# Kernel tuning notes

Measured on AMD Instinct MI355X. Metric: run time of the kernel, lower is better.

## Reference

```python
import jax, jax.numpy as jnp
import numpy as np
from jax import lax

FI, FO, K, EPS = 512, 256, 3, 1e-06


def _fir_kernel(gain):
    f = jnp.array([1.0, 3.0, 3.0, 1.0], dtype=jnp.float32)
    f = f[None, :] * f[:, None]
    f = f / f.sum() * gain  # (4,4), symmetric so conv-vs-correlation flip is a no-op
    return f


def setup_inputs() -> dict:
    key = jax.random.key(0)
    k1, k2 = jax.random.split(key)
    x = jax.random.normal(k1, (8, FI, 64, 64), dtype=jnp.float32)
    w = jax.random.normal(k2, (1, FO, FI, K, K), dtype=jnp.float32)
    return {"x": x, "w": w}


def reference(x, w):
    w_scale = (FI * K * K) ** (-0.5)
    wm = w[0] * w_scale  # (fo, fi, k, k); per-sample scale is constant across batch
    demod = lax.rsqrt(jnp.sum(wm * wm, axis=(1, 2, 3)) + EPS)  # (fo,)
    wm = wm * demod[:, None, None, None]
    # torch conv_transpose2d(stride=2, padding=0) with weight (fi, fo, k, k) where
    # weight[i, o] = wm[o, i]  ==  dilated conv with kernel flip(wm) OIHW, pad k-1=2.
    kern = wm[:, :, ::-1, ::-1]
    y = lax.conv_general_dilated(
        x, kern, window_strides=(1, 1), padding=[(2, 2), (2, 2)],
        lhs_dilation=(2, 2), dimension_numbers=("NCHW", "OIHW", "NCHW"))
    # upFirDn2D with scale=2, conv_k=3: p=0 -> pad (1,1) both dims, filter gain 4
    f = _fir_kernel(4.0)
    C = y.shape[1]
    fk = jnp.broadcast_to(f[None, None], (C, 1, 4, 4))
    y = lax.conv_general_dilated(
        y, fk, window_strides=(1, 1), padding=[(1, 1), (1, 1)],
        feature_group_count=C, dimension_numbers=("NCHW", "OIHW", "NCHW"))
    return y  # (8, 256, 128, 128)
```

## Files before the change

kernel.cpp:

```cpp
#include <hip/hip_runtime.h>

typedef unsigned short u16;
typedef unsigned int u32;
typedef __attribute__((ext_vector_type(8))) short bf16x8;
typedef __attribute__((ext_vector_type(4))) float f32x4;

#define XP_BYTES 35684352
#define YB_BYTES 68714544
#define HY_OFF   (XP_BYTES + YB_BYTES)
#define WS_NEED  ((size_t)HY_OFF + 2359296)
#define CS 16776

__device__ inline u16 f2bf(float f) {
  union { float f; unsigned u; } v; v.f = f;
  unsigned r = v.u + 0x7fffu + ((v.u >> 16) & 1u);
  return (u16)(r >> 16);
}

__device__ inline void gl_lds16(const u16* g, u16* l) {
  __builtin_amdgcn_global_load_lds(
      (const __attribute__((address_space(1))) unsigned int*)g,
      (__attribute__((address_space(3))) unsigned int*)l, 16, 0, 0);
}

__global__ void xprep(const float* __restrict__ x, u16* __restrict__ xp) {
  __shared__ float tile[64 * 65];
  int bid = blockIdx.x;
  int cc = bid & 7, h = (bid >> 3) & 63, n = bid >> 9;
  int c0 = cc * 64;
  int t = threadIdx.x;
  const float* xb = x + ((size_t)(n * 512 + c0) * 64 + h) * 64;
  for (int r = 0; r < 16; ++r) {
    int flat = r * 256 + t;
    int ci = flat >> 6, w = flat & 63;
    tile[w * 65 + ci] = xb[(size_t)ci * 4096 + w];
  }
  __syncthreads();
  for (int r = 0; r < 8; ++r) {
    int flat = r * 256 + t;
    int pr = flat & 31;
    int w = flat >> 5;
    int ci = pr * 2;
    float v0 = tile[w * 65 + ci], v1 = tile[w * 65 + ci + 1];
    unsigned pk = (unsigned)f2bf(v0) | ((unsigned)f2bf(v1) << 16);
    int kcabs = cc * 2 + (ci >> 5);
    int chl = ci & 31;
    u16* dst = xp + (size_t)(n * 16 + kcabs) * 139392 +
               (size_t)((h + 1) * 66 + (w + 1)) * 32 + chl;
    *(unsigned*)dst = pk;
  }
  if (t < 64) {
    int seg = t >> 4;
    int colsel = (seg >> 1) ? 65 : 0;
    int pl = cc * 2 + (seg & 1);
    int ui = t & 15;
    u16* dst = xp + (size_t)(n * 16 + pl) * 139392 +
               (size_t)((h + 1) * 66 + colsel) * 32 + ui * 2;
    *(u32*)dst = 0u;
  }
  if (h == 0 || h == 63) {
    int rowbase = (h == 0) ? 0 : 65 * 66;
    for (int j = t; j < 2112; j += 256) {
      int seg = j >> 4;
      int ui = j & 15;
      int pl = cc * 2 + (seg & 1);
      int pos = seg >> 1;
      u16* dst = xp + (size_t)(n * 16 + pl) * 139392 +
                 (size_t)(rowbase + pos) * 32 + ui * 2;
      *(u32*)dst = 0u;
    }
  }
}

__global__ void wprep9(const float* __restrict__ w, u16* __restrict__ Hy) {
  __shared__ float wl[4608];
  __shared__ float red[256];
  int o = blockIdx.x, t = threadIdx.x;
  const float* wo = w + (size_t)o * 4608;
  float s = 0.f;
  for (int j = t; j < 4608; j += 256) { float v = wo[j]; wl[j] = v; s += v * v; }
  red[t] = s;
  __syncthreads();
  for (int st = 128; st; st >>= 1) { if (t < st) red[t] += red[t + st]; __syncthreads(); }
  float demod = rsqrtf(red[0] * (1.0f / 4608.0f) + 1e-6f);
  float scale = demod * 0.014731391274719739f;
  const int DY[9] = {0, 2, 0, 2, 0, 2, 1, 1, 1};
  const int DX[9] = {0, 0, 2, 2, 1, 1, 0, 2, 1};
  for (int i = t; i < 512; i += 256) {
    int kc = i >> 5, il = i & 31;
#pragma unroll
    for (int pl = 0; pl < 9; ++pl) {
      float g = wl[i * 9 + DY[pl] * 3 + DX[pl]] * scale;
      Hy[(size_t)(pl * 16 + kc) * 8192 + (size_t)o * 32 + il] = f2bf(g);
    }
  }
}

#define BARR() __builtin_amdgcn_s_barrier()
#define WAITL() do { asm volatile("s_waitcnt lgkmcnt(0)" ::: "memory"); __builtin_amdgcn_sched_barrier(0); } while (0)
#define WAITV2() do { asm volatile("s_waitcnt vmcnt(2)" ::: "memory"); __builtin_amdgcn_sched_barrier(0); } while (0)
#define WAITV0() do { asm volatile("s_waitcnt vmcnt(0)" ::: "memory"); __builtin_amdgcn_sched_barrier(0); } while (0)

__device__ __forceinline__ void rdA4(const u16* sb, int tib, int la, int grp, int wm,
                                     bf16x8 af[4]) {
#pragma unroll
  for (int ti = 0; ti < 4; ++ti) {
    int p = (tib + ti) * 16 + la;
    int slot = (wm * 4 + grp) ^ (p & 7);
    af[ti] = *(const bf16x8*)(sb + p * 64 + slot * 8);
  }
}

__device__ __forceinline__ void rdB2(const u16* sb, int njb, int la, int grp, int wn,
                                     bf16x8 bf[2]) {
#pragma unroll
  for (int nj = 0; nj < 2; ++nj) {
    int p = (njb + nj) * 16 + la;
    int slot = (wn * 4 + grp) ^ (p & 7);
    bf[nj] = *(const bf16x8*)(sb + 8192 + p * 64 + slot * 8);
  }
}

template <int MIB, int NJ0>
__device__ __forceinline__ void qm8(const bf16x8 af[4], const bf16x8 bf[2],
                                    f32x4 acc[8][4]) {
#pragma unroll
  for (int ti = 0; ti < 4; ++ti)
#pragma unroll
    for (int nj = 0; nj < 2; ++nj)
      acc[MIB + ti][NJ0 + nj] = __builtin_amdgcn_mfma_f32_16x16x32_bf16(
          af[ti], bf[nj], acc[MIB + ti][NJ0 + nj], 0, 0, 0);
}

__device__ __forceinline__ void stA1(const u16* __restrict__ xp, u16* d,
                                     int tile, int NK, u32 a,
                                     u32 adj1, u32 adj2, u32 adj3) {
  if (tile < NK) {
    int tap = tile >> 4;
    u32 ko = (u32)((tile & 15) * 139392);
    u32 adj = tap == 0 ? 0u : (tap == 1 ? adj1 : (tap == 2 ? adj2 : adj3));
    gl_lds16(xp + (a + ko - adj), d);
  }
}

__device__ __forceinline__ void stB1(const u16* __restrict__ hb, u16* d,
                                     int tile, int NK, u32 b) {
  if (tile < NK) {
    int tap = tile >> 4;
    u32 ko = (u32)(tap * 131072 + (tile & 15) * 8192);
    gl_lds16(hb + (b + ko), d);
  }
}

__global__ __launch_bounds__(256, 2) void conv_y(const u16* __restrict__ xp,
                                                 const u16* __restrict__ Hy,
                                                 u16* __restrict__ yb) {
  __shared__ __align__(16) u16 su[24576];

  int bid = blockIdx.x;
  int t = threadIdx.x;
  int wid = t >> 6, lane = t & 63;

  int img = bid & 7;
  int kk = bid >> 3;
  int mt, oh, Wp, CNT, NTAP, PB, PO, STLIM;
  u32 adj1 = 0, adj2 = 0, adj3 = 0;
  if (kk < 34)       { int k2 = kk;       mt = k2 >> 1; oh = k2 & 1; Wp = 66; CNT = 4290; NTAP = 4; PB = 0; PO = 0;     STLIM = 4296;
                       adj1 = 2112u; adj2 = 32u; adj3 = 2144u; }
  else if (kk < 68)  { int k2 = kk - 34;  mt = k2 >> 1; oh = k2 & 1; Wp = 64; CNT = 4160; NTAP = 2; PB = 4; PO = 4296;  STLIM = 4160;
                       adj1 = 2112u; }
  else if (kk < 102) { int k2 = kk - 68;  mt = k2 >> 1; oh = k2 & 1; Wp = 66; CNT = 4224; NTAP = 2; PB = 6; PO = 8456;  STLIM = 4224;
                       adj1 = 32u; }
  else               { int k2 = kk - 102; mt = k2 >> 1; oh = k2 & 1; Wp = 64; CNT = 4096; NTAP = 1; PB = 8; PO = 12680; STLIM = 4096; }

  int m0 = mt * 256;
  int o0 = oh * 128;
  int NK = NTAP * 16;
  int NITER = NTAP * 8;
  const u16* hb = Hy + (size_t)PB * 131072;

  int wm = wid >> 1, wn = wid & 1;
  int la = lane & 15, grp = lane >> 4;

  int tp = t >> 3, ts = t & 7;
  u32 gA[4], gBv[2];
  {
    u32 ib = (u32)img * 2230272u;
#pragma unroll
    for (int j = 0; j < 4; ++j) {
      int p = j * 32 + tp;
      int e = ts ^ (p & 7);
      int ii = (e >> 2) * 128 + p;
      int kc = e & 3;
      int m = m0 + ii;
      if (m > CNT - 1) m = CNT - 1;
      u32 a = (u32)m / (u32)Wp;
      u32 b = (u32)m - a * (u32)Wp;
      gA[j] = ib + ((a + 1) * 66 + (b + 1)) * 32 + kc * 8;
    }
#pragma unroll
    for (int j = 0; j < 2; ++j) {
      int p = j * 32 + tp;
      int e = ts ^ (p & 7);
      int ol = (e >> 2) * 64 + p;
      int kc = e & 3;
      gBv[j] = (u32)((o0 + ol) * 32 + kc * 8);
    }
  }
  int ws = wid * 512;

  f32x4 acc[8][4];
#pragma unroll
  for (int i = 0; i < 8; ++i)
#pragma unroll
    for (int j = 0; j < 4; ++j) acc[i][j] = (f32x4){0.f, 0.f, 0.f, 0.f};

  stB1(hb, su + 8192 + ws, 0, NK, gBv[0]);
  stB1(hb, su + 10240 + ws, 0, NK, gBv[1]);
  stA1(xp, su + 0 + ws, 0, NK, gA[0], adj1, adj2, adj3);
  stA1(xp, su + 2048 + ws, 0, NK, gA[1], adj1, adj2, adj3);
  stA1(xp, su + 4096 + ws, 0, NK, gA[2], adj1, adj2, adj3);
  stA1(xp, su + 6144 + ws, 0, NK, gA[3], adj1, adj2, adj3);
  stB1(hb, su + 20480 + ws, 1, NK, gBv[0]);
  stB1(hb, su + 22528 + ws, 1, NK, gBv[1]);
  WAITV2();
  BARR();

  bf16x8 afA[4], afB[4], bfA[2], bfB[2];

#pragma unroll 1
  for (int it = 0; it < NITER; ++it) {
    int t0 = 2 * it;
    bool more = (it + 1 < NITER);

    rdA4(su, 0, la, grp, wm, afA);
    rdB2(su, 0, la, grp, wn, bfA);
    stA1(xp, su + 12288 + ws, t0 + 1, NK, gA[0], adj1, adj2, adj3);
    stA1(xp, su + 14336 + ws, t0 + 1, NK, gA[1], adj1, adj2, adj3);
    BARR(); WAITL();
    __builtin_amdgcn_s_setprio(1); qm8<0, 0>(afA, bfA, acc); __builtin_amdgcn_s_setprio(0);
    BARR();
    rdB2(su, 2, la, grp, wn, bfB);
    stA1(xp, su + 16384 + ws, t0 + 1, NK, gA[2], adj1, adj2, adj3);
    stA1(xp, su + 18432 + ws, t0 + 1, NK, gA[3], adj1, adj2, adj3);
    BARR(); WAITL();
    __builtin_amdgcn_s_setprio(1); qm8<0, 2>(afA, bfB, acc); __builtin_amdgcn_s_setprio(0);
    BARR();
    rdA4(su, 4, la, grp, wm, afB);
    stB1(hb, su + 8192 + ws, t0 + 2, NK, gBv[0]);
    stB1(hb, su + 10240 + ws, t0 + 2, NK, gBv[1]);
    BARR(); WAITL();
    __builtin_amdgcn_s_setprio(1);
    qm8<4, 0>(afB, bfA, acc); qm8<4, 2>(afB, bfB, acc);
    __builtin_amdgcn_s_setprio(0);
    if (more) { WAITV2(); } else { WAITV0(); }
    BARR();
    rdA4(su + 12288, 0, la, grp, wm, afA);
    rdB2(su + 12288, 0, la, grp, wn, bfA);
    stA1(xp, su + 0 + ws, t0 + 2, NK, gA[0], adj1, adj2, adj3);
    stA1(xp, su + 2048 + ws, t0 + 2, NK, gA[1], adj1, adj2, adj3);
    BARR(); WAITL();
    __builtin_amdgcn_s_setprio(1); qm8<0, 0>(afA, bfA, acc); __builtin_amdgcn_s_setprio(0);
    BARR();
    rdB2(su + 12288, 2, la, grp, wn, bfB);
    stA1(xp, su + 4096 + ws, t0 + 2, NK, gA[2], adj1, adj2, adj3);
    stA1(xp, su + 6144 + ws, t0 + 2, NK, gA[3], adj1, adj2, adj3);
    BARR(); WAITL();
    __builtin_amdgcn_s_setprio(1); qm8<0, 2>(afA, bfB, acc); __builtin_amdgcn_s_setprio(0);
    BARR();
    rdA4(su + 12288, 4, la, grp, wm, afB);
    stB1(hb, su + 20480 + ws, t0 + 3, NK, gBv[0]);
    stB1(hb, su + 22528 + ws, t0 + 3, NK, gBv[1]);
    BARR(); WAITL();
    __builtin_amdgcn_s_setprio(1);
    qm8<4, 0>(afB, bfA, acc); qm8<4, 2>(afB, bfB, acc);
    __builtin_amdgcn_s_setprio(0);
    if (more) { WAITV2(); }
    BARR();
  }

  WAITV0();
  __syncthreads();
  u16* ybp = yb + 8;
#pragma unroll 1
  for (int r = 0; r < 2; ++r) {
    if (wn == r) {
#pragma unroll
      for (int nj = 0; nj < 4; ++nj) {
        int orl = nj * 16 + la;
        int x7 = orl & 7;
#pragma unroll
        for (int mi = 0; mi < 8; ++mi)
#pragma unroll
          for (int jp = 0; jp < 2; ++jp) {
            int ml = wm * 128 + mi * 16 + grp * 4 + jp * 2;
            u32 pk = (u32)f2bf(acc[mi][nj][jp * 2]) |
                     ((u32)f2bf(acc[mi][nj][jp * 2 + 1]) << 16);
            *(u32*)(su + orl * 256 + (((ml >> 3) ^ x7) * 8) + (ml & 7)) = pk;
          }
      }
    }
    __syncthreads();
    {
      int ol = t >> 2, s2 = t & 3;
      int og = o0 + r * 64 + ol;
      size_t gb = (size_t)(img * 256 + og) * CS + PO + m0;
      int x7 = ol & 7;
#pragma unroll
      for (int i = 0; i < 8; ++i) {
        int cidx = s2 * 8 + i;
        int m = cidx * 8;
        if (m0 + m < STLIM)
          *(bf16x8*)(ybp + gb + m) = *(const bf16x8*)(su + ol * 256 + ((cidx ^ x7) * 8));
      }
    }
    if (r == 0) __syncthreads();
  }
}

__global__ void fir2(const u16* __restrict__ yb, float* __restrict__ z) {
  int flat = blockIdx.x * 256 + threadIdx.x;
  int qh = flat & 15, phb = (flat >> 4) & 31, o = (flat >> 9) & 255, n = flat >> 17;
  const u16* cb = yb + 8 + (size_t)(n * 256 + o) * CS;
  int a0 = 2 * phb - 1;
  int b0 = 4 * qh - 1;

  float out[4][8];
#pragma unroll
  for (int i = 0; i < 4; ++i)
#pragma unroll
    for (int j = 0; j < 8; ++j) out[i][j] = 0.f;

  const int PO_[4] = {0, 4296, 8456, 12680};
  const int WP_[4] = {66, 64, 66, 64};
  const int HA_[4] = {65, 65, 64, 64};
  const int WB_[4] = {65, 64, 65, 64};

#pragma unroll
  for (int ph = 0; ph < 4; ++ph) {
    int rp = ph >> 1, rq = ph & 1;
    const u16* pb = cb + PO_[ph];
    float hcol[4][8];
#pragma unroll
    for (int la = 0; la < 4; ++la) {
      if (rp == 0 && la == 0) continue;
      int ag = a0 + la;
      bool rv = (ag >= 0) && (ag < HA_[ph]);
      const u16* rb = pb + (ag * WP_[ph] + b0 - 1);
      u32 ls[4];
      ls[0] = *(const u32*)(rb);
      ls[1] = *(const u32*)(rb + 2);
      ls[2] = *(const u32*)(rb + 4);
      ls[3] = *(const u32*)(rb + 6);
      float v[6];
#pragma unroll
      for (int lb = 0; lb < 6; ++lb) {
        int jj = lb + 1;
        u32 w16 = (jj & 1) ? (ls[jj >> 1] >> 16) : (ls[jj >> 1] & 0xffffu);
        float fv = __uint_as_float(w16 << 16);
        int bg = b0 + lb;
        bool ok = rv && (bg >= 0) && (bg < WB_[ph]);
        v[lb] = ok ? fv : 0.f;
      }
#pragma unroll
      for (int e = 0; e < 4; ++e) {
        if (rq == 0) {
          hcol[la][2 * e]     = 3.f * v[e + 1] + v[e + 2];
          hcol[la][2 * e + 1] = v[e + 1] + 3.f * v[e + 2];
        } else {
          hcol[la][2 * e]     = v[e] + 3.f * v[e + 1];
          hcol[la][2 * e + 1] = 3.f * v[e + 1] + v[e + 2];
        }
      }
    }
#pragma unroll
    for (int jq = 0; jq < 8; ++jq) {
      if (rp == 0) {
        out[0][jq] += 3.f * hcol[1][jq] + hcol[2][jq];
        out[1][jq] += hcol[1][jq] + 3.f * hcol[2][jq];
        out[2][jq] += 3.f * hcol[2][jq] + hcol[3][jq];
        out[3][jq] += hcol[2][jq] + 3.f * hcol[3][jq];
      } else {
        out[0][jq] += hcol[0][jq] + 3.f * hcol[1][jq];
        out[1][jq] += 3.f * hcol[1][jq] + hcol[2][jq];
        out[2][jq] += hcol[1][jq] + 3.f * hcol[2][jq];
        out[3][jq] += 3.f * hcol[2][jq] + hcol[3][jq];
      }
    }
  }

  float* zb = z + ((size_t)(n * 256 + o) * 128 + phb * 4) * 128 + qh * 8;
#pragma unroll
  for (int ip = 0; ip < 4; ++ip) {
    f32x4 v0, v1;
#pragma unroll
    for (int j = 0; j < 4; ++j) { v0[j] = out[ip][j] * 0.0625f; v1[j] = out[ip][j + 4] * 0.0625f; }
    *(f32x4*)(zb + (size_t)ip * 128) = v0;
    *(f32x4*)(zb + (size_t)ip * 128 + 4) = v1;
  }
}

__global__ void xprep_flat(const float* __restrict__ x, u16* __restrict__ xp) {
  __shared__ float tile[64 * 65];
  int bid = blockIdx.x;
  int cc = bid & 7, h = (bid >> 3) & 63, n = bid >> 9;
  int c0 = cc * 64;
  int t = threadIdx.x;
  const float* xb = x + ((size_t)(n * 512 + c0) * 64 + h) * 64;
  for (int r = 0; r < 16; ++r) {
    int flat = r * 256 + t;
    int ci = flat >> 6, w = flat & 63;
    tile[w * 65 + ci] = xb[(size_t)ci * 4096 + w];
  }
  __syncthreads();
  u16* xpb = xp + ((size_t)(n * 66 + h + 1) * 66 + 1) * 512 + c0;
  for (int r = 0; r < 8; ++r) {
    int flat = r * 256 + t;
    int pr = flat & 31;
    int w = flat >> 5;
    int ci = pr * 2;
    float v0 = tile[w * 65 + ci], v1 = tile[w * 65 + ci + 1];
    unsigned pk = (unsigned)f2bf(v0) | ((unsigned)f2bf(v1) << 16);
    *(unsigned*)(xpb + (size_t)w * 512 + ci) = pk;
  }
  u16* rowbase = xp + ((size_t)(n * 66 + h + 1) * 66) * 512 + c0;
  if (t < 32) *(u32*)(rowbase + 2 * t) = 0u;
  else if (t < 64) *(u32*)(rowbase + (size_t)65 * 512 + 2 * (t - 32)) = 0u;
  if (h == 0) {
    u16* r0 = xp + ((size_t)(n * 66) * 66) * 512 + c0;
    for (int j = t; j < 2112; j += 256) {
      int col = j >> 5, wi = j & 31;
      *(u32*)(r0 + (size_t)col * 512 + 2 * wi) = 0u;
    }
  }
  if (h == 63) {
    u16* r65 = xp + ((size_t)(n * 66 + 65) * 66) * 512 + c0;
    for (int j = t; j < 2112; j += 256) {
      int col = j >> 5, wi = j & 31;
      *(u32*)(r65 + (size_t)col * 512 + 2 * wi) = 0u;
    }
  }
}

__global__ void wprep36(const float* __restrict__ w, u16* __restrict__ Hm) {
  __shared__ float wl[4608];
  __shared__ float red[256];
  int o = blockIdx.x, t = threadIdx.x;
  const float* wo = w + (size_t)o * 4608;
  float s = 0.f;
  for (int j = t; j < 4608; j += 256) { float v = wo[j]; wl[j] = v; s += v * v; }
  red[t] = s;
  __syncthreads();
  for (int st = 128; st; st >>= 1) { if (t < st) red[t] += red[t + st]; __syncthreads(); }
  float demod = rsqrtf(red[0] * (1.0f / 4608.0f) + 1e-6f);
  float scale = demod * 0.014731391274719739f;
  const float F1[4] = {1.f, 3.f, 3.f, 1.f};
  for (int i = t; i < 512; i += 256) {
    float wm[9];
    for (int k = 0; k < 9; ++k) wm[k] = wl[i * 9 + k] * scale;
    for (int rp = 0; rp < 2; ++rp)
      for (int rq = 0; rq < 2; ++rq)
        for (int u = 0; u < 3; ++u)
          for (int v = 0; v < 3; ++v) {
            int s_ = 2 - 2 * u + rp, t_ = 2 - 2 * v + rq;
            float g = 0.f;
            for (int dy = 0; dy < 3; ++dy) {
              int a = dy + 1 - s_;
              if (a < 0 || a > 3) continue;
              for (int dx = 0; dx < 3; ++dx) {
                int b = dx + 1 - t_;
                if (b < 0 || b > 3) continue;
                g += wm[dy * 3 + dx] * (F1[a] * F1[b]);
              }
            }
            g *= 0.0625f;
            Hm[(size_t)((rp * 2 + rq) * 9 + u * 3 + v) * 131072 + (size_t)o * 512 + i] = f2bf(g);
          }
  }
}

__global__ __launch_bounds__(256) void conv_main(const u16* __restrict__ xp,
                                                 const u16* __restrict__ Hm,
                                                 float* __restrict__ z) {
  __shared__ __align__(16) float smemf[8448];
  u16* su = (u16*)smemf;
  int bid = blockIdx.x;
  int sub = bid & 7;
  int rp = sub >> 2;
  int o0 = (sub & 3) * 64;
  int mtile = bid >> 3;
  int n_img = mtile >> 5;
  int hp0 = (mtile & 31) * 2;
  int t = threadIdx.x;
  int wave = t >> 6, lane = t & 63;
  int wm0 = (wave & 1) * 64;
  int wn0 = (wave >> 1) * 32;
  int la = lane & 15;
  int ks = (lane >> 4) * 8;
  int rsel = t >> 2;
  int koff = (t & 3) * 8;
  f32x4 acc[2][4][2];
#pragma unroll
  for (int a = 0; a < 2; ++a)
#pragma unroll
    for (int b = 0; b < 4; ++b)
#pragma unroll
      for (int c = 0; c < 2; ++c)
        acc[a][b][c] = (f32x4){0.f, 0.f, 0.f, 0.f};
#pragma unroll 1
  for (int tap = 0; tap < 9; ++tap) {
    int du = tap / 3, dv = tap - du * 3;
    const u16* gA0 = xp + ((size_t)(n_img * 66 + hp0 + du) * 66 + dv) * 512;
    const u16* gB0 = Hm + (size_t)(rp * 18 + tap) * 131072 + (size_t)(o0 + rsel) * 512 + koff;
    const u16* gAr0 = gA0 + (size_t)rsel * 512 + koff;
    const u16* gAr1 = gA0 + (size_t)(66 + rsel) * 512 + koff;
#pragma unroll 1
    for (int kc = 0; kc < 16; ++kc) {
      int c0 = kc * 32;
      __syncthreads();
      gl_lds16(gAr0 + c0, su + wave * 512);
      gl_lds16(gAr1 + c0, su + 2048 + wave * 512);
      gl_lds16(gB0 + c0,              su + 4096 + wave * 512);
      gl_lds16(gB0 + 9 * 131072 + c0, su + 6144 + wave * 512);
      __syncthreads();
      bf16x8 af[4];
#pragma unroll
      for (int ti = 0; ti < 4; ++ti)
        af[ti] = *(const bf16x8*)(su + (wm0 + ti * 16 + la) * 32 + ks);
      bf16x8 bfr[2][2];
#pragma unroll
      for (int rqq = 0; rqq < 2; ++rqq)
#pragma unroll
        for (int tj = 0; tj < 2; ++tj)
          bfr[rqq][tj] = *(const bf16x8*)(su + 4096 + rqq * 2048 + (wn0 + tj * 16 + la) * 32 + ks);
#pragma unroll
      for (int rqq = 0; rqq < 2; ++rqq)
#pragma unroll
        for (int ti = 0; ti < 4; ++ti)
#pragma unroll
          for (int tj = 0; tj < 2; ++tj)
            acc[rqq][ti][tj] = __builtin_amdgcn_mfma_f32_16x16x32_bf16(
                af[ti], bfr[rqq][tj], acc[rqq][ti][tj], 0, 0, 0);
    }
  }
  __syncthreads();
  float* lws = smemf + wave * 2112;
  int p = 2 * (hp0 + (wave & 1)) + rp;
#pragma unroll
  for (int tj = 0; tj < 2; ++tj) {
#pragma unroll
    for (int rqq = 0; rqq < 2; ++rqq)
#pragma unroll
      for (int ti = 0; ti < 4; ++ti) {
        int wqb = ti * 16 + (lane >> 4) * 4;
        f32x4 v = acc[rqq][ti][tj];
#pragma unroll
        for (int r = 0; r < 4; ++r)
          lws[la * 132 + 2 * (wqb + r) + rqq] = v[r];
      }
    __syncthreads();
    int obase = o0 + wn0 + tj * 16;
#pragma unroll
    for (int c = 0; c < 8; ++c) {
      int idx = c * 64 + lane;
      int ol = idx >> 5, q4 = (idx & 31) * 4;
      f32x4 vv = *(const f32x4*)(lws + ol * 132 + q4);
      *(f32x4*)(z + (((size_t)n_img * 256 + obase + ol) * 128 + p) * 128 + q4) = vv;
    }
    __syncthreads();
  }
}

extern "C" void kernel_launch(void* const* d_in, const int* in_sizes, int n_in,
                              void* d_out, int out_size, void* d_ws, size_t ws_size,
                              hipStream_t stream) {
  const float* x = (const float*)d_in[0];
  const float* w = (const float*)d_in[1];
  float* z = (float*)d_out;
  u16* xp = (u16*)d_ws;

  if (ws_size >= WS_NEED) {
    u16* yb = (u16*)((char*)d_ws + XP_BYTES);
    u16* hy = (u16*)((char*)d_ws + HY_OFF);
    xprep<<<4096, 256, 0, stream>>>(x, xp);
    wprep9<<<256, 256, 0, stream>>>(w, hy);
    conv_y<<<1072, 256, 0, stream>>>(xp, hy, yb);
    fir2<<<4096, 256, 0, stream>>>(yb, z);
  } else {
    u16* Hm = (u16*)((char*)d_ws + XP_BYTES);
    hipMemsetAsync(xp, 0, XP_BYTES, stream);
    xprep_flat<<<4096, 256, 0, stream>>>(x, xp);
    wprep36<<<256, 256, 0, stream>>>(w, Hm);
    conv_main<<<2048, 256, 0, stream>>>(xp, Hm, z);
  }
}
```

Before: 312.6 us.

## Replace fine-grained double-buffered GEMM loop with triple-buffered prefetch-two pipeline

The conv GEMM main loop moves from a two-buffer schedule with many sub-phase barriers, LDS waits and setprio toggles to a three-stage ring buffer. Each iteration issues loads two tiles ahead, reads all fragments for the current tile and runs 32 MFMAs with a single wait and barrier. This removes most barrier and lgkm-wait overhead and deepens the global-load prefetch. In exchange LDS use rises from 48KB to 72KB per block, which may limit the two-blocks-per-CU occupancy, and the fragment registers held live grow.

```diff
diff --git a/kernel.cpp b/kernel.cpp
--- a/kernel.cpp
+++ b/kernel.cpp
@@ -97,8 +97,7 @@
 }
 
 #define BARR() __builtin_amdgcn_s_barrier()
-#define WAITL() do { asm volatile("s_waitcnt lgkmcnt(0)" ::: "memory"); __builtin_amdgcn_sched_barrier(0); } while (0)
-#define WAITV2() do { asm volatile("s_waitcnt vmcnt(2)" ::: "memory"); __builtin_amdgcn_sched_barrier(0); } while (0)
+#define WAITV6() do { asm volatile("s_waitcnt vmcnt(6)" ::: "memory"); __builtin_amdgcn_sched_barrier(0); } while (0)
 #define WAITV0() do { asm volatile("s_waitcnt vmcnt(0)" ::: "memory"); __builtin_amdgcn_sched_barrier(0); } while (0)
 
 __device__ __forceinline__ void rdA4(const u16* sb, int tib, int la, int grp, int wm,
@@ -119,17 +118,6 @@
     int slot = (wn * 4 + grp) ^ (p & 7);
     bf[nj] = *(const bf16x8*)(sb + 8192 + p * 64 + slot * 8);
   }
-}
-
-template <int MIB, int NJ0>
-__device__ __forceinline__ void qm8(const bf16x8 af[4], const bf16x8 bf[2],
-                                    f32x4 acc[8][4]) {
-#pragma unroll
-  for (int ti = 0; ti < 4; ++ti)
-#pragma unroll
-    for (int nj = 0; nj < 2; ++nj)
-      acc[MIB + ti][NJ0 + nj] = __builtin_amdgcn_mfma_f32_16x16x32_bf16(
-          af[ti], bf[nj], acc[MIB + ti][NJ0 + nj], 0, 0, 0);
 }
 
 __device__ __forceinline__ void stA1(const u16* __restrict__ xp, u16* d,
@@ -155,7 +143,7 @@
 __global__ __launch_bounds__(256, 2) void conv_y(const u16* __restrict__ xp,
                                                  const u16* __restrict__ Hy,
                                                  u16* __restrict__ yb) {
-  __shared__ __align__(16) u16 su[24576];
+  __shared__ __align__(16) u16 su[36864];
 
   int bid = blockIdx.x;
   int t = threadIdx.x;
@@ -176,7 +164,6 @@
   int m0 = mt * 256;
   int o0 = oh * 128;
   int NK = NTAP * 16;
-  int NITER = NTAP * 8;
   const u16* hb = Hy + (size_t)PB * 131072;
 
   int wm = wid >> 1, wn = wid & 1;
@@ -221,65 +208,47 @@
   stA1(xp, su + 2048 + ws, 0, NK, gA[1], adj1, adj2, adj3);
   stA1(xp, su + 4096 + ws, 0, NK, gA[2], adj1, adj2, adj3);
   stA1(xp, su + 6144 + ws, 0, NK, gA[3], adj1, adj2, adj3);
-  stB1(hb, su + 20480 + ws, 1, NK, gBv[0]);
-  stB1(hb, su + 22528 + ws, 1, NK, gBv[1]);
-  WAITV2();
+  stB1(hb, su + 12288 + 8192 + ws, 1, NK, gBv[0]);
+  stB1(hb, su + 12288 + 10240 + ws, 1, NK, gBv[1]);
+  stA1(xp, su + 12288 + 0 + ws, 1, NK, gA[0], adj1, adj2, adj3);
+  stA1(xp, su + 12288 + 2048 + ws, 1, NK, gA[1], adj1, adj2, adj3);
+  stA1(xp, su + 12288 + 4096 + ws, 1, NK, gA[2], adj1, adj2, adj3);
+  stA1(xp, su + 12288 + 6144 + ws, 1, NK, gA[3], adj1, adj2, adj3);
+  WAITV6();
   BARR();
 
-  bf16x8 afA[4], afB[4], bfA[2], bfB[2];
-
+  int cur = 0;
 #pragma unroll 1
-  for (int it = 0; it < NITER; ++it) {
-    int t0 = 2 * it;
-    bool more = (it + 1 < NITER);
-
-    rdA4(su, 0, la, grp, wm, afA);
-    rdB2(su, 0, la, grp, wn, bfA);
-    stA1(xp, su + 12288 + ws, t0 + 1, NK, gA[0], adj1, adj2, adj3);
-    stA1(xp, su + 14336 + ws, t0 + 1, NK, gA[1], adj1, adj2, adj3);
-    BARR(); WAITL();
-    __builtin_amdgcn_s_setprio(1); qm8<0, 0>(afA, bfA, acc); __builtin_amdgcn_s_setprio(0);
+  for (int tt = 0; tt < NK; ++tt) {
+    const u16* sb = su + cur * 12288;
+    int st2 = cur + 2; if (st2 >= 3) st2 -= 3;
+    u16* sd = su + st2 * 12288 + ws;
+
+    bf16x8 af[8], bf[4];
+    rdA4(sb, 0, la, grp, wm, af + 0);
+    rdB2(sb, 0, la, grp, wn, bf + 0);
+    rdB2(sb, 2, la, grp, wn, bf + 2);
+    rdA4(sb, 4, la, grp, wm, af + 4);
+
+    stA1(xp, sd + 0, tt + 2, NK, gA[0], adj1, adj2, adj3);
+    stA1(xp, sd + 2048, tt + 2, NK, gA[1], adj1, adj2, adj3);
+    stA1(xp, sd + 4096, tt + 2, NK, gA[2], adj1, adj2, adj3);
+    stA1(xp, sd + 6144, tt + 2, NK, gA[3], adj1, adj2, adj3);
+    stB1(hb, sd + 8192, tt + 2, NK, gBv[0]);
+    stB1(hb, sd + 10240, tt + 2, NK, gBv[1]);
+
+#pragma unroll
+    for (int ti = 0; ti < 8; ++ti)
+#pragma unroll
+      for (int nj = 0; nj < 4; ++nj)
+        acc[ti][nj] = __builtin_amdgcn_mfma_f32_16x16x32_bf16(
+            af[ti], bf[nj], acc[ti][nj], 0, 0, 0);
+
+    if (tt + 2 < NK) { WAITV6(); } else { WAITV0(); }
     BARR();
-    rdB2(su, 2, la, grp, wn, bfB);
-    stA1(xp, su + 16384 + ws, t0 + 1, NK, gA[2], adj1, adj2, adj3);
-    stA1(xp, su + 18432 + ws, t0 + 1, NK, gA[3], adj1, adj2, adj3);
-    BARR(); WAITL();
-    __builtin_amdgcn_s_setprio(1); qm8<0, 2>(afA, bfB, acc); __builtin_amdgcn_s_setprio(0);
-    BARR();
-    rdA4(su, 4, la, grp, wm, afB);
-    stB1(hb, su + 8192 + ws, t0 + 2, NK, gBv[0]);
-    stB1(hb, su + 10240 + ws, t0 + 2, NK, gBv[1]);
-    BARR(); WAITL();
-    __builtin_amdgcn_s_setprio(1);
-    qm8<4, 0>(afB, bfA, acc); qm8<4, 2>(afB, bfB, acc);
-    __builtin_amdgcn_s_setprio(0);
-    if (more) { WAITV2(); } else { WAITV0(); }
-    BARR();
-    rdA4(su + 12288, 0, la, grp, wm, afA);
-    rdB2(su + 12288, 0, la, grp, wn, bfA);
-    stA1(xp, su + 0 + ws, t0 + 2, NK, gA[0], adj1, adj2, adj3);
-    stA1(xp, su + 2048 + ws, t0 + 2, NK, gA[1], adj1, adj2, adj3);
-    BARR(); WAITL();
-    __builtin_amdgcn_s_setprio(1); qm8<0, 0>(afA, bfA, acc); __builtin_amdgcn_s_setprio(0);
-    BARR();
-    rdB2(su + 12288, 2, la, grp, wn, bfB);
-    stA1(xp, su + 4096 + ws, t0 + 2, NK, gA[2], adj1, adj2, adj3);
-    stA1(xp, su + 6144 + ws, t0 + 2, NK, gA[3], adj1, adj2, adj3);
-    BARR(); WAITL();
-    __builtin_amdgcn_s_setprio(1); qm8<0, 2>(afA, bfB, acc); __builtin_amdgcn_s_setprio(0);
-    BARR();
-    rdA4(su + 12288, 4, la, grp, wm, afB);
-    stB1(hb, su + 20480 + ws, t0 + 3, NK, gBv[0]);
-    stB1(hb, su + 22528 + ws, t0 + 3, NK, gBv[1]);
-    BARR(); WAITL();
-    __builtin_amdgcn_s_setprio(1);
-    qm8<4, 0>(afB, bfA, acc); qm8<4, 2>(afB, bfB, acc);
-    __builtin_amdgcn_s_setprio(0);
-    if (more) { WAITV2(); }
-    BARR();
-  }
-
-  WAITV0();
+    cur = cur + 1; if (cur >= 3) cur -= 3;
+  }
+
   __syncthreads();
   u16* ybp = yb + 8;
 #pragma unroll 1
```

After: 306.4 us. 2.0% less time.
